# Performance work log

Hardware: AMD Instinct MI355X
Metric: run time of the kernel (lower is better)

Reference implementation:

```python
import jax, jax.numpy as jnp
import numpy as np

# module init constants
HEAVY_RATIO = 0.1
RECENT_RATIO = 0.1


def setup_inputs() -> dict:
    key = jax.random.key(0)
    attn_weights = jax.random.normal(key, (2, 32, 1024, 1024), dtype=jnp.float32)
    return {"attn_weights": attn_weights, "group_size": 8}


def reference(attn_weights, group_size):
    # First-forward path of CachedHeavyRecentAttentionMasker (cached_indices is None).
    bs, head, q_len, k_len = attn_weights.shape
    dtype = attn_weights.dtype
    min_value = jnp.finfo(dtype).min
    num_groups = head // group_size

    # [bs, ng, gs, q, k]
    attn_g = attn_weights.reshape(bs, num_groups, group_size, q_len, k_len)
    tmp_attn = jax.nn.softmax(attn_g.astype(jnp.float32), axis=-1).astype(dtype)
    importance = tmp_attn.sum(axis=-2)  # [bs, ng, gs, k]

    heavy_budget = max(1, min(int(HEAVY_RATIO * k_len), k_len))
    _, topk_idx = jax.lax.top_k(importance, heavy_budget)  # [bs, ng, gs, hb]
    # scatter True at topk indices -> boolean heavy mask per head
    heavy_mask_head = jnp.any(jax.nn.one_hot(topk_idx, k_len, dtype=jnp.bool_), axis=-2)  # [bs, ng, gs, k]
    heavy_mask_group = jnp.any(heavy_mask_head, axis=2)  # [bs, ng, k]

    # first call: final mask is just the heavy-hitter group mask
    final_mask_group = heavy_mask_group

    i = jnp.arange(q_len)[:, None]
    j = jnp.arange(k_len)[None, :]
    causal = j <= i  # [q, k]
    recent_budget = int(RECENT_RATIO * k_len)
    if recent_budget > 0:
        recent_band = causal & (j >= i - recent_budget)
    else:
        recent_band = i == j

    # broadcast group mask to per-head [bs, head, q, k]
    keep = jnp.broadcast_to(
        final_mask_group[:, :, None, None, :],
        (bs, num_groups, group_size, q_len, k_len),
    ).reshape(bs, head, q_len, k_len)
    keep = (keep & causal) | recent_band

    fetch_mask = jnp.where(keep, jnp.zeros((), dtype), jnp.full((), min_value, dtype))
    density = keep.sum().astype(jnp.float32) / (bs * head) / (q_len * (q_len + 1) / 2)
    return fetch_mask, density
```

## Files before the change

kernel.cpp:

```cpp
#include <hip/hip_runtime.h>
#include <float.h>
#include <stdint.h>

#define QLEN 1024
#define KLEN 1024
#define NHEADS 64
#define NGROUPS 8
#define CH 16
#define HEAVY_BUDGET 102
#define RECENT 102
#define RECENT_SUM 100219LL

#define MASK_VAL __uint_as_float(0xFF7F0000u)

typedef float v4f __attribute__((ext_vector_type(4)));
typedef unsigned long long u64;
typedef unsigned long long v2u __attribute__((ext_vector_type(2)));


#define WS_NEED (73728u + (size_t)NHEADS * CH * KLEN * 4u)

#define PARTIAL_F  0
#define HEADMASK_F (NHEADS * CH * KLEN)
#define HEAVY_F    (HEADMASK_F + (NHEADS * KLEN) / 4)
#define GCOUNT_F   (HEAVY_F + (NGROUPS * KLEN) / 4)
#define TAIL_LO    1040
#define TAIL_HI    1042

template <bool WM>
__global__ __launch_bounds__(256) void k_importance(const float* __restrict__ attn,
                                                    float* __restrict__ partial,
                                                    float* __restrict__ out) {
  const int blk   = blockIdx.x;
  const int head  = blk >> 4;
  const int chunk = blk & (CH - 1);
  const int tid   = threadIdx.x;
  const int wave  = tid >> 6;
  const int lane  = tid & 63;

  float acc[16];
#pragma unroll
  for (int t = 0; t < 16; ++t) acc[t] = 0.f;

  const v4f* head4 = (const v4f*)(attn + (size_t)head * QLEN * KLEN);
  const int q0 = chunk * (QLEN / CH) + wave * 16;

  v4f a[4], b[4];
  {
    const v4f* rowA = head4 + (size_t)q0 * (KLEN / 4);
    const v4f* rowB = rowA + (KLEN / 4);
#pragma unroll
    for (int c = 0; c < 4; ++c) { a[c] = rowA[c * 64 + lane]; b[c] = rowB[c * 64 + lane]; }
  }

  for (int rp = 0; rp < 8; ++rp) {
    v4f na[4], nb[4];
    if (rp < 7) {
      const v4f* nA = head4 + (size_t)(q0 + 2 * rp + 2) * (KLEN / 4);
      const v4f* nB = nA + (KLEN / 4);
#pragma unroll
      for (int c = 0; c < 4; ++c) { na[c] = nA[c * 64 + lane]; nb[c] = nB[c * 64 + lane]; }
    }

    float za = 0.f, zb = 0.f;
#pragma unroll
    for (int c = 0; c < 4; ++c)
#pragma unroll
      for (int d = 0; d < 4; ++d) {
        a[c][d] = __expf(a[c][d]);
        b[c][d] = __expf(b[c][d]);
        za += a[c][d];
        zb += b[c][d];
      }

#pragma unroll
    for (int s = 32; s >= 1; s >>= 1) {
      za += __shfl_xor(za, s, 64);
      zb += __shfl_xor(zb, s, 64);
    }

    const float iza = 1.0f / za, izb = 1.0f / zb;
#pragma unroll
    for (int c = 0; c < 4; ++c)
#pragma unroll
      for (int d = 0; d < 4; ++d)
        acc[c * 4 + d] += a[c][d] * iza + b[c][d] * izb;

    if constexpr (WM) {
      const float mv = MASK_VAL;
#pragma unroll
      for (int rr = 0; rr < 2; ++rr) {
        const int i    = q0 + 2 * rp + rr;
        const int lo   = i - RECENT;
        const int nvec = (lo > 0) ? ((lo + 3) >> 2) : 0;
        v4f* rowOut = (v4f*)(out + ((size_t)head * QLEN + i) * KLEN);
#pragma unroll
        for (int c = 0; c < 4; ++c) {
          const int vidx = c * 64 + lane;
          if (vidx >= nvec) {
            const int k0 = vidx * 4;
            v4f o;
            o[0] = (k0 + 0 <= i) ? 0.f : mv;
            o[1] = (k0 + 1 <= i) ? 0.f : mv;
            o[2] = (k0 + 2 <= i) ? 0.f : mv;
            o[3] = (k0 + 3 <= i) ? 0.f : mv;
            __builtin_nontemporal_store(o, rowOut + vidx);
          }
        }
      }
    }

#pragma unroll
    for (int c = 0; c < 4; ++c) { a[c] = na[c]; b[c] = nb[c]; }
  }

  __shared__ float lds[4][KLEN];
#pragma unroll
  for (int c = 0; c < 4; ++c)
#pragma unroll
    for (int d = 0; d < 4; ++d)
      lds[wave][(c * 64 + lane) * 4 + d] = acc[c * 4 + d];
  __syncthreads();

  v4f* outp = (v4f*)(partial + ((size_t)head * CH + chunk) * KLEN);
  const int k0 = tid * 4;
  v4f o;
#pragma unroll
  for (int d = 0; d < 4; ++d)
    o[d] = (lds[0][k0 + d] + lds[1][k0 + d]) + (lds[2][k0 + d] + lds[3][k0 + d]);
  outp[tid] = o;
}

__global__ __launch_bounds__(256) void k_rank(const float* __restrict__ partial,
                                              unsigned char* __restrict__ head_mask) {
  const int head = blockIdx.x >> 2;
  const int seg  = blockIdx.x & 3;
  const int t    = threadIdx.x;

  __shared__ u64 keys[KLEN];

  const float* base = partial + (size_t)head * CH * KLEN;
#pragma unroll
  for (int j = 0; j < 4; ++j) {
    const int k = j * 256 + t;
    float s = 0.f;
#pragma unroll
    for (int c = 0; c < CH; ++c) s += base[c * KLEN + k];
    keys[k] = ((u64)__float_as_uint(s) << 10) | (u64)(KLEN - 1 - k);
  }
  __syncthreads();

  const int kk = seg * 256 + t;
  const u64 mykey = keys[kk];
  const v2u* k2 = (const v2u*)keys;
  int rank = 0;
#pragma unroll 8
  for (int u = 0; u < KLEN / 2; ++u) {
    const v2u w = k2[u];
    rank += (w[0] > mykey) ? 1 : 0;
    rank += (w[1] > mykey) ? 1 : 0;
  }
  head_mask[head * KLEN + kk] = (rank < HEAVY_BUDGET) ? 1 : 0;
}

__global__ __launch_bounds__(1024) void k_combine(const unsigned char* __restrict__ head_mask,
                                                  unsigned char* __restrict__ heavy,
                                                  long long* __restrict__ gcount) {
  const int grp = blockIdx.x;
  const int k   = threadIdx.x;

  unsigned char m = 0;
#pragma unroll
  for (int hh = 0; hh < 8; ++hh) m |= head_mask[(grp * 8 + hh) * KLEN + k];
  heavy[grp * KLEN + k] = m;

  const int umax = QLEN - 1 - (RECENT + 1);
  int contrib = (m && k <= umax) ? (umax + 1 - k) : 0;

  __shared__ int red[16];
  int sum = contrib;
#pragma unroll
  for (int s = 32; s >= 1; s >>= 1) sum += __shfl_xor(sum, s, 64);
  if ((k & 63) == 0) red[k >> 6] = sum;
  __syncthreads();
  if (k < 16) {
    int x = red[k];
#pragma unroll
    for (int s = 8; s >= 1; s >>= 1) x += __shfl_xor(x, s, 64);
    if (k == 0) gcount[grp] = 8LL * (RECENT_SUM + (long long)x);
  }
}

__global__ __launch_bounds__(256) void k_fix(const unsigned char* __restrict__ heavy,
                                             const long long* __restrict__ gcount,
                                             float* __restrict__ out) {
  const int tid  = threadIdx.x;
  const int row0 = blockIdx.x * 8;
  const int grp  = row0 >> 13;
  const float mv = MASK_VAL;

  if (blockIdx.x == 0 && tid == 0) {
    long long s = 0;
    for (int g = 0; g < NGROUPS; ++g) s += gcount[g];
    float f = (float)s;
    f = f / 64.0f;
    f = f / 524800.0f;
    out[(size_t)NHEADS * QLEN * KLEN] = f;
  }

  const uchar4 hv = ((const uchar4*)(heavy + grp * KLEN))[tid];
  const int j0 = tid * 4;

#pragma unroll
  for (int r = 0; r < 8; ++r) {
    const int row = row0 + r;
    const int i   = row & (QLEN - 1);
    const int lo  = i - RECENT;
    const int nvec = (lo > 0) ? ((lo + 3) >> 2) : 0;
    if (tid < nvec) {
      v4f o;
      o[0] = ((j0 + 0) <= i && (hv.x || (j0 + 0) >= lo)) ? 0.f : mv;
      o[1] = ((j0 + 1) <= i && (hv.y || (j0 + 1) >= lo)) ? 0.f : mv;
      o[2] = ((j0 + 2) <= i && (hv.z || (j0 + 2) >= lo)) ? 0.f : mv;
      o[3] = ((j0 + 3) <= i && (hv.w || (j0 + 3) >= lo)) ? 0.f : mv;
      __builtin_nontemporal_store(o, (v4f*)(out + (size_t)row * KLEN) + tid);
    }
  }
}

__global__ __launch_bounds__(256) void k_mask_full(const unsigned char* __restrict__ heavy,
                                                   float* __restrict__ out) {
  const int tid  = threadIdx.x;
  const int row0 = blockIdx.x * 8;
  const int grp  = row0 >> 13;
  const float mv = MASK_VAL;
  const uchar4 hv = ((const uchar4*)(heavy + grp * KLEN))[tid];
  const int hx = hv.x, hy = hv.y, hz = hv.z, hw = hv.w;
  const int j0 = tid * 4;

#pragma unroll
  for (int r = 0; r < 8; ++r) {
    const int row = row0 + r;
    if (row >= TAIL_LO && row <= TAIL_HI) continue;
    const int i  = row & (QLEN - 1);
    const int lo = i - RECENT;
    v4f o;
    o[0] = ((j0 + 0) <= i && (hx || (j0 + 0) >= lo)) ? 0.f : mv;
    o[1] = ((j0 + 1) <= i && (hy || (j0 + 1) >= lo)) ? 0.f : mv;
    o[2] = ((j0 + 2) <= i && (hz || (j0 + 2) >= lo)) ? 0.f : mv;
    o[3] = ((j0 + 3) <= i && (hw || (j0 + 3) >= lo)) ? 0.f : mv;
    __builtin_nontemporal_store(o, (v4f*)(out + (size_t)row * KLEN) + tid);
  }
}

__global__ __launch_bounds__(256) void k_tail(const long long* __restrict__ gcount,
                                              float* __restrict__ out) {
  const int tid = threadIdx.x;
  const float mv = MASK_VAL;

  float dens = 0.f;
  if (tid == 0) {
    long long s = 0;
    for (int g = 0; g < NGROUPS; ++g) s += gcount[g];
    float f = (float)s;
    f = f / 64.0f;
    f = f / 524800.0f;
    dens = f;
  }
  __syncthreads();

  const int j0 = tid * 4;
  for (int row = TAIL_LO; row <= TAIL_HI; ++row) {
    const int i = row & (QLEN - 1);
    v4f o;
    o[0] = ((j0 + 0) <= i) ? 0.f : mv;
    o[1] = ((j0 + 1) <= i) ? 0.f : mv;
    o[2] = ((j0 + 2) <= i) ? 0.f : mv;
    o[3] = ((j0 + 3) <= i) ? 0.f : mv;
    ((v4f*)(out + (size_t)row * KLEN))[tid] = o;
  }
  if (tid == 0) out[(size_t)NHEADS * QLEN * KLEN] = dens;
}

extern "C" void kernel_launch(void* const* d_in, const int* in_sizes, int n_in,
                              void* d_out, int out_size, void* d_ws, size_t ws_size,
                              hipStream_t stream) {
  const float* attn = (const float*)d_in[0];
  float* out = (float*)d_out;
  char*  ws  = (char*)d_ws;

  if (ws && ws_size >= WS_NEED) {
    long long*     gcount    = (long long*)(ws + 64);
    unsigned char* heavy     = (unsigned char*)(ws + 128);
    unsigned char* head_mask = (unsigned char*)(ws + 8320);
    float*         partial   = (float*)(ws + 73728);

    k_importance<true><<<NHEADS * CH, 256, 0, stream>>>(attn, partial, out);
    k_rank<<<NHEADS * 4, 256, 0, stream>>>(partial, head_mask);
    k_combine<<<NGROUPS, 1024, 0, stream>>>(head_mask, heavy, gcount);
    k_fix<<<8192, 256, 0, stream>>>(heavy, gcount, out);
  } else {
    float*         partial   = out + PARTIAL_F;
    unsigned char* head_mask = (unsigned char*)(out + HEADMASK_F);
    unsigned char* heavy     = (unsigned char*)(out + HEAVY_F);
    long long*     gcount    = (long long*)(out + GCOUNT_F);

    k_importance<false><<<NHEADS * CH, 256, 0, stream>>>(attn, partial, nullptr);
    k_rank<<<NHEADS * 4, 256, 0, stream>>>(partial, head_mask);
    k_combine<<<NGROUPS, 1024, 0, stream>>>(head_mask, heavy, gcount);
    k_mask_full<<<8192, 256, 0, stream>>>(heavy, out);
    k_tail<<<1, 256, 0, stream>>>(gcount, out);
  }
}
```

Before: 128.0 us.

## Move mask writes out of importance kernel into single full mask pass

Stops the importance kernel from writing the causal/recent part of the output mask while it streams the input, and has the final mask kernel write every element of each row instead. This lightens the compute-heavy importance kernel and removes its output-store traffic from overlapping with input reads. In exchange the last kernel writes the full 256 MB output alone, which loses the overlap of stores with the read-bound phase.

```diff
diff --git a/kernel.cpp b/kernel.cpp
--- a/kernel.cpp
+++ b/kernel.cpp
@@ -17,7 +17,6 @@
 typedef unsigned long long u64;
 typedef unsigned long long v2u __attribute__((ext_vector_type(2)));
 
-
 #define WS_NEED (73728u + (size_t)NHEADS * CH * KLEN * 4u)
 
 #define PARTIAL_F  0
@@ -27,10 +26,8 @@
 #define TAIL_LO    1040
 #define TAIL_HI    1042
 
-template <bool WM>
 __global__ __launch_bounds__(256) void k_importance(const float* __restrict__ attn,
-                                                    float* __restrict__ partial,
-                                                    float* __restrict__ out) {
+                                                    float* __restrict__ partial) {
   const int blk   = blockIdx.x;
   const int head  = blk >> 4;
   const int chunk = blk & (CH - 1);
@@ -85,30 +82,6 @@
 #pragma unroll
       for (int d = 0; d < 4; ++d)
         acc[c * 4 + d] += a[c][d] * iza + b[c][d] * izb;
-
-    if constexpr (WM) {
-      const float mv = MASK_VAL;
-#pragma unroll
-      for (int rr = 0; rr < 2; ++rr) {
-        const int i    = q0 + 2 * rp + rr;
-        const int lo   = i - RECENT;
-        const int nvec = (lo > 0) ? ((lo + 3) >> 2) : 0;
-        v4f* rowOut = (v4f*)(out + ((size_t)head * QLEN + i) * KLEN);
-#pragma unroll
-        for (int c = 0; c < 4; ++c) {
-          const int vidx = c * 64 + lane;
-          if (vidx >= nvec) {
-            const int k0 = vidx * 4;
-            v4f o;
-            o[0] = (k0 + 0 <= i) ? 0.f : mv;
-            o[1] = (k0 + 1 <= i) ? 0.f : mv;
-            o[2] = (k0 + 2 <= i) ? 0.f : mv;
-            o[3] = (k0 + 3 <= i) ? 0.f : mv;
-            __builtin_nontemporal_store(o, rowOut + vidx);
-          }
-        }
-      }
-    }
 
 #pragma unroll
     for (int c = 0; c < 4; ++c) { a[c] = na[c]; b[c] = nb[c]; }
@@ -191,9 +164,9 @@
   }
 }
 
-__global__ __launch_bounds__(256) void k_fix(const unsigned char* __restrict__ heavy,
-                                             const long long* __restrict__ gcount,
-                                             float* __restrict__ out) {
+__global__ __launch_bounds__(256) void k_mask(const unsigned char* __restrict__ heavy,
+                                              const long long* __restrict__ gcount,
+                                              float* __restrict__ out) {
   const int tid  = threadIdx.x;
   const int row0 = blockIdx.x * 8;
   const int grp  = row0 >> 13;
@@ -209,26 +182,24 @@
   }
 
   const uchar4 hv = ((const uchar4*)(heavy + grp * KLEN))[tid];
+  const int hx = hv.x, hy = hv.y, hz = hv.z, hw = hv.w;
   const int j0 = tid * 4;
 
 #pragma unroll
   for (int r = 0; r < 8; ++r) {
     const int row = row0 + r;
-    const int i   = row & (QLEN - 1);
-    const int lo  = i - RECENT;
-    const int nvec = (lo > 0) ? ((lo + 3) >> 2) : 0;
-    if (tid < nvec) {
-      v4f o;
-      o[0] = ((j0 + 0) <= i && (hv.x || (j0 + 0) >= lo)) ? 0.f : mv;
-      o[1] = ((j0 + 1) <= i && (hv.y || (j0 + 1) >= lo)) ? 0.f : mv;
-      o[2] = ((j0 + 2) <= i && (hv.z || (j0 + 2) >= lo)) ? 0.f : mv;
-      o[3] = ((j0 + 3) <= i && (hv.w || (j0 + 3) >= lo)) ? 0.f : mv;
-      __builtin_nontemporal_store(o, (v4f*)(out + (size_t)row * KLEN) + tid);
-    }
-  }
-}
-
-__global__ __launch_bounds__(256) void k_mask_full(const unsigned char* __restrict__ heavy,
+    const int i  = row & (QLEN - 1);
+    const int lo = i - RECENT;
+    v4f o;
+    o[0] = ((j0 + 0) <= i && (hx || (j0 + 0) >= lo)) ? 0.f : mv;
+    o[1] = ((j0 + 1) <= i && (hy || (j0 + 1) >= lo)) ? 0.f : mv;
+    o[2] = ((j0 + 2) <= i && (hz || (j0 + 2) >= lo)) ? 0.f : mv;
+    o[3] = ((j0 + 3) <= i && (hw || (j0 + 3) >= lo)) ? 0.f : mv;
+    __builtin_nontemporal_store(o, (v4f*)(out + (size_t)row * KLEN) + tid);
+  }
+}
+
+__global__ __launch_bounds__(256) void k_mask_skip(const unsigned char* __restrict__ heavy,
                                                    float* __restrict__ out) {
   const int tid  = threadIdx.x;
   const int row0 = blockIdx.x * 8;
@@ -295,20 +266,20 @@
     unsigned char* head_mask = (unsigned char*)(ws + 8320);
     float*         partial   = (float*)(ws + 73728);
 
-    k_importance<true><<<NHEADS * CH, 256, 0, stream>>>(attn, partial, out);
+    k_importance<<<NHEADS * CH, 256, 0, stream>>>(attn, partial);
     k_rank<<<NHEADS * 4, 256, 0, stream>>>(partial, head_mask);
     k_combine<<<NGROUPS, 1024, 0, stream>>>(head_mask, heavy, gcount);
-    k_fix<<<8192, 256, 0, stream>>>(heavy, gcount, out);
+    k_mask<<<8192, 256, 0, stream>>>(heavy, gcount, out);
   } else {
     float*         partial   = out + PARTIAL_F;
     unsigned char* head_mask = (unsigned char*)(out + HEADMASK_F);
     unsigned char* heavy     = (unsigned char*)(out + HEAVY_F);
     long long*     gcount    = (long long*)(out + GCOUNT_F);
 
-    k_importance<false><<<NHEADS * CH, 256, 0, stream>>>(attn, partial, nullptr);
+    k_importance<<<NHEADS * CH, 256, 0, stream>>>(attn, partial);
     k_rank<<<NHEADS * 4, 256, 0, stream>>>(partial, head_mask);
     k_combine<<<NGROUPS, 1024, 0, stream>>>(head_mask, heavy, gcount);
-    k_mask_full<<<8192, 256, 0, stream>>>(heavy, out);
+    k_mask_skip<<<8192, 256, 0, stream>>>(heavy, out);
     k_tail<<<1, 256, 0, stream>>>(gcount, out);
   }
 }
```

Result: faster. 114.1 us (-10.8%).
